# Kernel optimization log

Measured on AMD Instinct MI355X. Metric: run time of the kernel, lower is better.

## Reference

```python
import jax, jax.numpy as jnp
import numpy as np

E = 1024
H = 16
N, S, T = 4, 2048, 2048


def setup_inputs() -> dict:
    key = jax.random.key(0)
    ks = jax.random.split(key, 11)
    scale = 1.0 / np.sqrt(E)
    inp = {
        "query": jax.random.normal(ks[0], (N, S, E), jnp.float32),
        "key": jax.random.normal(ks[1], (N, T, E), jnp.float32),
        "value": jax.random.normal(ks[2], (N, T, E), jnp.float32),
        "Wq": jax.random.normal(ks[3], (E, E), jnp.float32) * scale,
        "bq": jax.random.normal(ks[4], (E,), jnp.float32) * 0.01,
        "Wk": jax.random.normal(ks[5], (E, E), jnp.float32) * scale,
        "bk": jax.random.normal(ks[6], (E,), jnp.float32) * 0.01,
        "Wv": jax.random.normal(ks[7], (E, E), jnp.float32) * scale,
        "bv": jax.random.normal(ks[8], (E,), jnp.float32) * 0.01,
        "Wp": jax.random.normal(ks[9], (E, E), jnp.float32) * scale,
        "bp": jax.random.normal(ks[10], (E,), jnp.float32) * 0.01,
    }
    return inp


def reference(query, key, value, Wq, bq, Wk, bk, Wv, bv, Wp, bp):
    n, s, e = query.shape
    t = value.shape[1]
    hd = e // H
    # Linear projections (torch Linear: x @ W^T + b), split into heads -> [N,H,S,hd]
    Q = (query @ Wq.T + bq).reshape(n, s, H, hd).transpose(0, 2, 1, 3)
    K = (key @ Wk.T + bk).reshape(n, t, H, hd).transpose(0, 2, 1, 3)
    V = (value @ Wv.T + bv).reshape(n, t, H, hd).transpose(0, 2, 1, 3)
    scale = 1.0 / jnp.sqrt(jnp.asarray(hd, Q.dtype))
    attn = jnp.einsum("nhsd,nhtd->nhst", Q, K) * scale  # [N,H,S,T]
    A = jax.nn.softmax(attn, axis=-1)
    Y = jnp.einsum("nhst,nhtd->nhsd", A, V)  # [N,H,S,hd]
    Y = Y.transpose(0, 2, 1, 3).reshape(n, s, e)
    return Y @ Wp.T + bp
```

## Files before the change

kernel.cpp:

```cpp
#include <hip/hip_runtime.h>
#include <hip/hip_bf16.h>
#include <stdint.h>


#define E_DIM 1024
#define H_NUM 16
#define HD 64
#define NB 4
#define SEQ 2048
#define NTOK (NB * SEQ)

typedef __bf16 bf16x8 __attribute__((ext_vector_type(8)));
typedef float f32x4 __attribute__((ext_vector_type(4)));
typedef float f32x16 __attribute__((ext_vector_type(16)));
typedef unsigned short u16;

#define MFMA16(a, b, c) __builtin_amdgcn_mfma_f32_16x16x32_bf16(a, b, c, 0, 0, 0)
#define MFMA32(a, b, c) __builtin_amdgcn_mfma_f32_32x32x16_bf16(a, b, c, 0, 0, 0)

#define VMCNT(n) asm volatile("s_waitcnt vmcnt(" #n ")" ::: "memory")
#define BAR() __builtin_amdgcn_s_barrier()
#define PRIO1() __builtin_amdgcn_s_setprio(1)
#define PRIO0() __builtin_amdgcn_s_setprio(0)

__device__ __forceinline__ u16 f2bf(float f) {
  unsigned int u = __builtin_bit_cast(unsigned int, f);
  unsigned int r = (u + 0x7FFFu + ((u >> 16) & 1u)) >> 16;
  return (u16)r;
}

__device__ __forceinline__ float fexp2(float x) {
  return __builtin_amdgcn_exp2f(x);
}

__device__ __forceinline__ void gload_lds16(const void* g, void* l) {
  __builtin_amdgcn_global_load_lds((const __attribute__((address_space(1))) void*)g,
                                   (__attribute__((address_space(3))) void*)l,
                                   16, 0, 0);
}

__device__ __forceinline__ unsigned cvtpk(float lo, float hi2) {
  unsigned w;
  asm("v_cvt_pk_bf16_f32 %0, %1, %2" : "=v"(w) : "v"(lo), "v"(hi2));
  return w;
}
__device__ __forceinline__ void plswap(unsigned& a, unsigned& b) {
  asm("v_permlane32_swap_b32 %0, %1" : "+v"(a), "+v"(b));
}

__global__ __launch_bounds__(256) void cvt7(const float* __restrict__ s0,
                                            const float* __restrict__ s1,
                                            const float* __restrict__ s2,
                                            const float* __restrict__ s3,
                                            const float* __restrict__ s4,
                                            const float* __restrict__ s5,
                                            const float* __restrict__ s6,
                                            u16* d0, u16* d1, u16* d2, u16* d3,
                                            u16* d4, u16* d5, u16* d6,
                                            int nbig, int nsmall) {
  const int t = blockIdx.y;
  const float* in;
  u16* out;
  int n4;
  switch (t) {
    case 0: in = s0; out = d0; n4 = nbig; break;
    case 1: in = s1; out = d1; n4 = nbig; break;
    case 2: in = s2; out = d2; n4 = nbig; break;
    case 3: in = s3; out = d3; n4 = nsmall; break;
    case 4: in = s4; out = d4; n4 = nsmall; break;
    case 5: in = s5; out = d5; n4 = nsmall; break;
    default: in = s6; out = d6; n4 = nsmall; break;
  }
  int idx = blockIdx.x * 256 + threadIdx.x;
  int stride = gridDim.x * 256;
  for (int i = idx; i < n4; i += stride) {
    float4 v = ((const float4*)in)[i];
    ushort4 o;
    o.x = f2bf(v.x); o.y = f2bf(v.y); o.z = f2bf(v.z); o.w = f2bf(v.w);
    ((ushort4*)out)[i] = o;
  }
}


__device__ __forceinline__ void rdA(bf16x8 (&af)[4][2], const char* pA, int off) {
#pragma unroll
  for (int mi = 0; mi < 4; mi++)
#pragma unroll
    for (int kk = 0; kk < 2; kk++)
      af[mi][kk] = *(const bf16x8*)(pA + off + mi * 2048 + kk * 64);
}
__device__ __forceinline__ void rdB(bf16x8 (&bfr)[2][2], const char* pB, int off) {
#pragma unroll
  for (int nj = 0; nj < 2; nj++)
#pragma unroll
    for (int kk = 0; kk < 2; kk++)
      bfr[nj][kk] = *(const bf16x8*)(pB + off + nj * 2048 + kk * 64);
}
template <int MI0, int NJ0>
__device__ __forceinline__ void mm16(f32x4 (&acc)[8][4], bf16x8 (&af)[4][2],
                                     bf16x8 (&bfr)[2][2]) {
#pragma unroll
  for (int kk = 0; kk < 2; kk++)
#pragma unroll
    for (int mi = 0; mi < 4; mi++)
#pragma unroll
      for (int nj = 0; nj < 2; nj++)
        acc[MI0 + mi][NJ0 + nj] = MFMA16(af[mi][kk], bfr[nj][kk], acc[MI0 + mi][NJ0 + nj]);
}

__global__ void __launch_bounds__(512, 2) gemm_qkv8(
    const u16* __restrict__ qb, const u16* __restrict__ kb, const u16* __restrict__ vb,
    const u16* __restrict__ Wcat, const float* __restrict__ bq,
    const float* __restrict__ bk, const float* __restrict__ bv,
    u16* __restrict__ Qp, u16* __restrict__ Kp, u16* __restrict__ Vt, float qscale) {
  extern __shared__ char LDS[];
  const int tid = threadIdx.x;
  const int w = tid >> 6, l = tid & 63;
  const int lr = l & 15, lg = l >> 4;
  const int wr = w >> 2, wc2 = w & 3;
  const int m0 = blockIdx.y * 256;
  const int n0g = blockIdx.x * 256;
  const int z = blockIdx.x >> 2;
  const u16* A = (z == 0) ? qb : (z == 1) ? kb : vb;

  const int colsw = (lg << 4) ^ ((lr & 4) << 3);
  const char* pA = LDS + (wr * 16384 + lr * 128 + colsw);
  const char* pB = LDS + (65536 + (wc2 >> 1) * 16384 + ((wc2 & 1) * 64 + lr) * 128 + colsw);

  const int sr0 = tid >> 3;
  const int sc = (((tid & 7) * 16) ^ ((sr0 & 4) << 3)) >> 1;
  const u16* aS[2];
  const u16* bS[2];
#pragma unroll
  for (int ld = 0; ld < 2; ld++) {
    aS[ld] = A + (size_t)(m0 + ld * 64 + sr0) * E_DIM + sc;
    bS[ld] = Wcat + (size_t)(n0g + ld * 64 + sr0) * E_DIM + sc;
  }

#define STG_A(h, kt)                                                                   \
  do {                                                                                 \
    const int _b = (kt) & 1;                                                           \
    gload_lds16(aS[0] + (h) * 131072 + (size_t)(kt) * 64,                              \
                LDS + _b * 32768 + (h) * 16384 + w * 1024);                            \
    gload_lds16(aS[1] + (h) * 131072 + (size_t)(kt) * 64,                              \
                LDS + _b * 32768 + (h) * 16384 + w * 1024 + 8192);                     \
  } while (0)
#define STG_B(h, kt)                                                                   \
  do {                                                                                 \
    const int _b = (kt) & 1;                                                           \
    gload_lds16(bS[0] + (h) * 131072 + (size_t)(kt) * 64,                              \
                LDS + 65536 + _b * 32768 + (h) * 16384 + w * 1024);                    \
    gload_lds16(bS[1] + (h) * 131072 + (size_t)(kt) * 64,                              \
                LDS + 65536 + _b * 32768 + (h) * 16384 + w * 1024 + 8192);             \
  } while (0)

  f32x4 acc[8][4] = {};
  bf16x8 af[4][2], bfr[2][2];

#define FRAME(T, LAST)                                                                 \
  do {                                                                                 \
                                                             \
    rdA(af, pA, 0); rdB(bfr, pB, 0);                                                   \
    STG_B(0, (T) + 1);                                                                 \
    BAR(); PRIO1(); mm16<0, 0>(acc, af, bfr); PRIO0(); BAR();                          \
                                                                     \
    rdB(bfr, pB, 4096);                                                                \
    STG_B(1, (T) + 1);                                                                 \
    BAR(); PRIO1(); mm16<0, 2>(acc, af, bfr); PRIO0(); BAR();                          \
                                                                     \
    rdA(af, pA, 8192);                                                                 \
    STG_A(1, (T) + 1);                                                                 \
    BAR(); PRIO1(); mm16<4, 2>(acc, af, bfr); PRIO0(); BAR();                          \
                                                             \
    rdB(bfr, pB, 0);                                                                   \
    if (!(LAST)) { STG_A(0, (T) + 2); VMCNT(2); } else { VMCNT(0); }                   \
    BAR(); PRIO1(); mm16<4, 0>(acc, af, bfr); PRIO0(); BAR();                          \
                                                     \
    rdA(af, pA, 32768); rdB(bfr, pB, 32768);                                           \
    if (!(LAST)) STG_B(0, (T) + 2);                                                    \
    BAR(); PRIO1(); mm16<0, 0>(acc, af, bfr); PRIO0(); BAR();                          \
                                                                     \
    rdB(bfr, pB, 32768 + 4096);                                                        \
    if (!(LAST)) STG_B(1, (T) + 2);                                                    \
    BAR(); PRIO1(); mm16<0, 2>(acc, af, bfr); PRIO0(); BAR();                          \
                                                                     \
    rdA(af, pA, 32768 + 8192);                                                         \
    if (!(LAST)) STG_A(1, (T) + 2);                                                    \
    BAR(); PRIO1(); mm16<4, 2>(acc, af, bfr); PRIO0(); BAR();                          \
                                                             \
    rdB(bfr, pB, 32768);                                                               \
    if (!(LAST)) { STG_A(0, (T) + 3); VMCNT(2); }                                      \
    BAR(); PRIO1(); mm16<4, 0>(acc, af, bfr); PRIO0(); BAR();                          \
  } while (0)

  STG_A(0, 0); STG_A(1, 0); STG_B(0, 0); STG_B(1, 0); STG_A(0, 1);
  VMCNT(2);
  BAR();

#pragma unroll 1
  for (int T = 0; T < 14; T += 2) FRAME(T, false);
  FRAME(14, true);

  const float* bias = (z == 0) ? bq : (z == 1) ? bk : bv;
  const float osc = (z == 0) ? qscale : 1.0f;
#pragma unroll
  for (int mi = 0; mi < 8; mi++) {
#pragma unroll
    for (int nj = 0; nj < 4; nj++) {
      const int colm = (n0g + wc2 * 64 + nj * 16 + lr) & 1023;
      const float bvv = bias[colm];
      const int row0 = m0 + wr * 128 + mi * 16 + lg * 4;
      if (z == 2) {
        const int nb = row0 >> 11, t = row0 & (SEQ - 1);
        const int hh = colm >> 6, d = colm & 63;
        ushort4 o;
        o.x = f2bf(acc[mi][nj][0] + bvv);
        o.y = f2bf(acc[mi][nj][1] + bvv);
        o.z = f2bf(acc[mi][nj][2] + bvv);
        o.w = f2bf(acc[mi][nj][3] + bvv);
        *(ushort4*)&Vt[(((size_t)((nb * H_NUM + hh) * HD + d)) << 11) + t] = o;
      } else {
        u16* Cb = (z == 0) ? Qp : Kp;
#pragma unroll
        for (int ri = 0; ri < 4; ri++)
          Cb[(size_t)(row0 + ri) * E_DIM + colm] = f2bf((acc[mi][nj][ri] + bvv) * osc);
      }
    }
  }
#undef FRAME
#undef STG_A
#undef STG_B
}

__global__ __launch_bounds__(256) void gemm_proj(const u16* __restrict__ A,
                                                 const u16* __restrict__ W,
                                                 const float* __restrict__ bias,
                                                 float* __restrict__ Cout) {
  __shared__ u16 As[2][128 * 32];
  __shared__ u16 Bs[2][128 * 32];
  const int tid = threadIdx.x;
  const int w = tid >> 6, l = tid & 63;
  const int lg = l >> 4, lr = l & 15;
  const int m0 = blockIdx.y * 128, n0 = blockIdx.x * 128;
  const int wr = (w >> 1) * 64, wc = (w & 1) * 64;
  f32x4 acc[4][4] = {};
  const int qa0 = w, qa1 = 4 + w;
  const int rowA0 = qa0 * 16 + (l >> 2), rowA1 = qa1 * 16 + (l >> 2);
  const int colA = (l & 3) * 8;
  const u16* aptr0 = A + (size_t)(m0 + rowA0) * E_DIM + colA;
  const u16* aptr1 = A + (size_t)(m0 + rowA1) * E_DIM + colA;
  const u16* bptr0 = W + (size_t)(n0 + rowA0) * E_DIM + colA;
  const u16* bptr1 = W + (size_t)(n0 + rowA1) * E_DIM + colA;

#define GSTAGE(B, k0)                                   \
  do {                                                  \
    gload_lds16(aptr0 + (k0), &As[B][qa0 * 512]);       \
    gload_lds16(aptr1 + (k0), &As[B][qa1 * 512]);       \
    gload_lds16(bptr0 + (k0), &Bs[B][qa0 * 512]);       \
    gload_lds16(bptr1 + (k0), &Bs[B][qa1 * 512]);       \
  } while (0)
#define GBODY(B)                                                          \
  do {                                                                    \
    bf16x8 af[4], bfr[4];                                                 \
    _Pragma("unroll") for (int mi = 0; mi < 4; mi++)                      \
      af[mi] = *(const bf16x8*)&As[B][(wr + mi * 16 + lr) * 32 + lg * 8]; \
    _Pragma("unroll") for (int nj = 0; nj < 4; nj++)                      \
      bfr[nj] = *(const bf16x8*)&Bs[B][(wc + nj * 16 + lr) * 32 + lg * 8];\
    _Pragma("unroll") for (int mi = 0; mi < 4; mi++)                      \
      _Pragma("unroll") for (int nj = 0; nj < 4; nj++)                    \
        acc[mi][nj] = MFMA16(af[mi], bfr[nj], acc[mi][nj]);               \
  } while (0)

  GSTAGE(0, 0);
  __syncthreads();
#pragma unroll 1
  for (int k0 = 0; k0 < E_DIM; k0 += 64) {
    GSTAGE(1, k0 + 32);
    GBODY(0);
    __syncthreads();
    if (k0 + 64 < E_DIM) GSTAGE(0, k0 + 64);
    GBODY(1);
    __syncthreads();
  }
#pragma unroll
  for (int mi = 0; mi < 4; mi++) {
#pragma unroll
    for (int nj = 0; nj < 4; nj++) {
      const int col = n0 + wc + nj * 16 + lr;
      const float bv = bias[col];
      const int row0 = m0 + wr + mi * 16 + lg * 4;
#pragma unroll
      for (int ri = 0; ri < 4; ri++)
        Cout[(size_t)(row0 + ri) * E_DIM + col] = acc[mi][nj][ri] + bv;
    }
  }
#undef GSTAGE
#undef GBODY
}

__global__ __launch_bounds__(256) void attn_kernel(const u16* __restrict__ Qp,
                                                   const u16* __restrict__ Kp,
                                                   const u16* __restrict__ Vt,
                                                   u16* __restrict__ Yb) {
  __shared__ u16 Ks[2][64 * 64];
  __shared__ u16 Vs[2][64 * 64];
  const int h = blockIdx.x, qt = blockIdx.y, n = blockIdx.z;
  const int tid = threadIdx.x;
  const int w = tid >> 6, l = tid & 63;
  const int c = l & 31, hi = l >> 5;
  const int q0 = qt * 128 + w * 32;

  bf16x8 qf[4];
  {
    const u16* qrow = Qp + (size_t)(n * SEQ + q0 + c) * E_DIM + h * HD + hi * 8;
#pragma unroll
    for (int ks = 0; ks < 4; ks++) qf[ks] = *(const bf16x8*)(qrow + ks * 16);
  }

  f32x16 y0 = {}, y1 = {};
  float lrun = 0.f;

  int lo[4];
#pragma unroll
  for (int ks = 0; ks < 4; ks++)
    lo[ks] = c * 128 + ((ks * 32 + hi * 16) ^ ((c & 7) << 4));

  const int sr = l >> 3;
  const int sc = ((l & 7) ^ sr) * 8;
  const u16* kgb[2];
  const u16* vgb[2];
#pragma unroll
  for (int g = 0; g < 2; g++) {
    const int row_ = (w << 4) + (g << 3) + sr;
    kgb[g] = Kp + (size_t)(n * SEQ + row_) * E_DIM + h * HD + sc;
    vgb[g] = Vt + ((size_t)((n * H_NUM + h) * HD + row_)) * SEQ + sc;
  }

#define STAGE(B, t0)                                                    \
  do {                                                                  \
    gload_lds16(kgb[0] + (size_t)(t0) * E_DIM, &Ks[B][(w << 10)]);      \
    gload_lds16(kgb[1] + (size_t)(t0) * E_DIM, &Ks[B][(w << 10) + 512]);\
    gload_lds16(vgb[0] + (t0), &Vs[B][(w << 10)]);                      \
    gload_lds16(vgb[1] + (t0), &Vs[B][(w << 10) + 512]);                \
  } while (0)

#define TILE_BODY(B)                                                           \
  do {                                                                         \
    const char* kb = (const char*)Ks[B];                                       \
    const char* vb = (const char*)Vs[B];                                       \
    f32x16 s0 = {}, s1 = {};                                                   \
    PRIO1();                                                                   \
    _Pragma("unroll") for (int ks = 0; ks < 4; ks++) {                         \
      bf16x8 ka0 = *(const bf16x8*)(kb + lo[ks]);                              \
      bf16x8 ka1 = *(const bf16x8*)(kb + lo[ks] + 4096);                       \
      s0 = MFMA32(ka0, qf[ks], s0);                                            \
      s1 = MFMA32(ka1, qf[ks], s1);                                            \
    }                                                                          \
    PRIO0();                                                                   \
    float p0 = 0.f, p1 = 0.f, p2 = 0.f, p3 = 0.f;                              \
    _Pragma("unroll") for (int r = 0; r < 4; r++) {                            \
      s0[r] = fexp2(s0[r]);         p0 += s0[r];                               \
      s0[r + 4] = fexp2(s0[r + 4]); p1 += s0[r + 4];                           \
      s0[r + 8] = fexp2(s0[r + 8]); p2 += s0[r + 8];                           \
      s0[r + 12] = fexp2(s0[r + 12]); p3 += s0[r + 12];                        \
    }                                                                          \
    _Pragma("unroll") for (int r = 0; r < 4; r++) {                            \
      s1[r] = fexp2(s1[r]);         p0 += s1[r];                               \
      s1[r + 4] = fexp2(s1[r + 4]); p1 += s1[r + 4];                           \
      s1[r + 8] = fexp2(s1[r + 8]); p2 += s1[r + 8];                           \
      s1[r + 12] = fexp2(s1[r + 12]); p3 += s1[r + 12];                        \
    }                                                                          \
    lrun += (p0 + p1) + (p2 + p3);                                             \
    PRIO1();                                                                   \
    _Pragma("unroll") for (int ks = 0; ks < 4; ks++) {                         \
      const f32x16 pe = (ks < 2) ? s0 : s1;                                    \
      const int b0 = (ks & 1) * 8;                                             \
      unsigned wa = cvtpk(pe[b0 + 0], pe[b0 + 1]);                             \
      unsigned wb = cvtpk(pe[b0 + 4], pe[b0 + 5]);                             \
      unsigned wc2 = cvtpk(pe[b0 + 2], pe[b0 + 3]);                            \
      unsigned wd = cvtpk(pe[b0 + 6], pe[b0 + 7]);                             \
      plswap(wa, wb);                                                          \
      plswap(wc2, wd);                                                         \
      union { unsigned u[4]; bf16x8 v; } pa;                                   \
      pa.u[0] = wa; pa.u[1] = wc2; pa.u[2] = wb; pa.u[3] = wd;                 \
      bf16x8 va0 = *(const bf16x8*)(vb + lo[ks]);                              \
      bf16x8 va1 = *(const bf16x8*)(vb + lo[ks] + 4096);                       \
      y0 = MFMA32(va0, pa.v, y0);                                              \
      y1 = MFMA32(va1, pa.v, y1);                                              \
    }                                                                          \
    PRIO0();                                                                   \
  } while (0)

  STAGE(0, 0);
  __syncthreads();

#pragma unroll 1
  for (int it = 0; it < SEQ / 64; it += 2) {
    STAGE(1, (it + 1) * 64);
    TILE_BODY(0);
    __syncthreads();
    if (it + 2 < SEQ / 64) STAGE(0, (it + 2) * 64);
    TILE_BODY(1);
    __syncthreads();
  }

  lrun += __shfl_xor(lrun, 32, 64);
  const float inv = 1.f / lrun;
  u16* orow = Yb + (size_t)(n * SEQ + q0 + c) * E_DIM + h * HD;
#pragma unroll
  for (int df = 0; df < 2; df++) {
    const f32x16 yy = df ? y1 : y0;
#pragma unroll
    for (int g = 0; g < 4; g++) {
      ushort4 o;
      o.x = f2bf(yy[g * 4 + 0] * inv);
      o.y = f2bf(yy[g * 4 + 1] * inv);
      o.z = f2bf(yy[g * 4 + 2] * inv);
      o.w = f2bf(yy[g * 4 + 3] * inv);
      *(ushort4*)(orow + df * 32 + g * 8 + hi * 4) = o;
    }
  }
#undef STAGE
#undef TILE_BODY
}

extern "C" void kernel_launch(void* const* d_in, const int* in_sizes, int n_in,
                              void* d_out, int out_size, void* d_ws, size_t ws_size,
                              hipStream_t stream) {
  const float* query = (const float*)d_in[0];
  const float* key   = (const float*)d_in[1];
  const float* value = (const float*)d_in[2];
  const float* Wq = (const float*)d_in[3];
  const float* bq = (const float*)d_in[4];
  const float* Wk = (const float*)d_in[5];
  const float* bk = (const float*)d_in[6];
  const float* Wv = (const float*)d_in[7];
  const float* bv = (const float*)d_in[8];
  const float* Wp = (const float*)d_in[9];
  const float* bp = (const float*)d_in[10];

  const size_t TOK_E = (size_t)NTOK * E_DIM;
  const size_t W_E = (size_t)E_DIM * E_DIM;

  u16* ws = (u16*)d_ws;
  u16* qb  = ws;
  u16* kb  = qb + TOK_E;
  u16* vb  = kb + TOK_E;
  u16* wqb = vb + TOK_E;
  u16* wkb = wqb + W_E;
  u16* wvb = wkb + W_E;
  u16* wpb = wvb + W_E;
  u16* Qp  = wpb + W_E;
  u16* Kp  = Qp + TOK_E;
  u16* Vtb = Kp + TOK_E;
  u16* Yb  = Vtb + TOK_E;

  cvt7<<<dim3(1024, 7), 256, 0, stream>>>(query, key, value, Wq, Wk, Wv, Wp,
                                          qb, kb, vb, wqb, wkb, wvb, wpb,
                                          (int)(TOK_E / 4), (int)(W_E / 4));

  const float sc2 = 0.125f * 1.44269504088896f;

  hipFuncSetAttribute((const void*)gemm_qkv8,
                      hipFuncAttributeMaxDynamicSharedMemorySize, 131072);
  gemm_qkv8<<<dim3(3072 / 256, NTOK / 256), 512, 131072, stream>>>(
      qb, kb, vb, wqb, bq, bk, bv, Qp, Kp, Vtb, sc2);

  attn_kernel<<<dim3(H_NUM, SEQ / 128, NB), 256, 0, stream>>>(Qp, Kp, Vtb, Yb);

  gemm_proj<<<dim3(E_DIM / 128, NTOK / 128), 256, 0, stream>>>(Yb, wpb, bp, (float*)d_out);
}
```

Measured before the change: 218.5 us.

## Process two 32-row query subtiles per wave in attention kernel to reuse K/V

Each wave in the attention kernel now handles 64 query rows, as two 32-row sets, instead of 32. Each K and V fragment read from LDS feeds four MFMAs instead of two, and the grid is halved to 256 queries per block. This halves LDS and global K/V traffic per query and amortizes staging and barriers. The cost is roughly double the accumulator registers, a launch bound of 2 blocks per CU, and fewer blocks (512) to spread across CUs, which may reduce occupancy.

```diff
diff --git a/kernel.cpp b/kernel.cpp
--- a/kernel.cpp
+++ b/kernel.cpp
@@ -46,6 +46,19 @@
 }
 __device__ __forceinline__ void plswap(unsigned& a, unsigned& b) {
   asm("v_permlane32_swap_b32 %0, %1" : "+v"(a), "+v"(b));
+}
+
+template <int B0>
+__device__ __forceinline__ bf16x8 packpa(const f32x16& pe) {
+  unsigned wa = cvtpk(pe[B0 + 0], pe[B0 + 1]);
+  unsigned wb = cvtpk(pe[B0 + 4], pe[B0 + 5]);
+  unsigned wc2 = cvtpk(pe[B0 + 2], pe[B0 + 3]);
+  unsigned wd = cvtpk(pe[B0 + 6], pe[B0 + 7]);
+  plswap(wa, wb);
+  plswap(wc2, wd);
+  union { unsigned u[4]; bf16x8 v; } pa;
+  pa.u[0] = wa; pa.u[1] = wc2; pa.u[2] = wb; pa.u[3] = wd;
+  return pa.v;
 }
 
 __global__ __launch_bounds__(256) void cvt7(const float* __restrict__ s0,
@@ -81,7 +94,6 @@
   }
 }
 
-
 __device__ __forceinline__ void rdA(bf16x8 (&af)[4][2], const char* pA, int off) {
 #pragma unroll
   for (int mi = 0; mi < 4; mi++)
@@ -159,35 +171,27 @@
 
 #define FRAME(T, LAST)                                                                 \
   do {                                                                                 \
-                                                             \
     rdA(af, pA, 0); rdB(bfr, pB, 0);                                                   \
     STG_B(0, (T) + 1);                                                                 \
     BAR(); PRIO1(); mm16<0, 0>(acc, af, bfr); PRIO0(); BAR();                          \
-                                                                     \
     rdB(bfr, pB, 4096);                                                                \
     STG_B(1, (T) + 1);                                                                 \
     BAR(); PRIO1(); mm16<0, 2>(acc, af, bfr); PRIO0(); BAR();                          \
-                                                                     \
     rdA(af, pA, 8192);                                                                 \
     STG_A(1, (T) + 1);                                                                 \
     BAR(); PRIO1(); mm16<4, 2>(acc, af, bfr); PRIO0(); BAR();                          \
-                                                             \
     rdB(bfr, pB, 0);                                                                   \
     if (!(LAST)) { STG_A(0, (T) + 2); VMCNT(2); } else { VMCNT(0); }                   \
     BAR(); PRIO1(); mm16<4, 0>(acc, af, bfr); PRIO0(); BAR();                          \
-                                                     \
     rdA(af, pA, 32768); rdB(bfr, pB, 32768);                                           \
     if (!(LAST)) STG_B(0, (T) + 2);                                                    \
     BAR(); PRIO1(); mm16<0, 0>(acc, af, bfr); PRIO0(); BAR();                          \
-                                                                     \
     rdB(bfr, pB, 32768 + 4096);                                                        \
     if (!(LAST)) STG_B(1, (T) + 2);                                                    \
     BAR(); PRIO1(); mm16<0, 2>(acc, af, bfr); PRIO0(); BAR();                          \
-                                                                     \
     rdA(af, pA, 32768 + 8192);                                                         \
     if (!(LAST)) STG_A(1, (T) + 2);                                                    \
     BAR(); PRIO1(); mm16<4, 2>(acc, af, bfr); PRIO0(); BAR();                          \
-                                                             \
     rdB(bfr, pB, 32768);                                                               \
     if (!(LAST)) { STG_A(0, (T) + 3); VMCNT(2); }                                      \
     BAR(); PRIO1(); mm16<4, 0>(acc, af, bfr); PRIO0(); BAR();                          \
@@ -298,27 +302,31 @@
 #undef GBODY
 }
 
-__global__ __launch_bounds__(256) void attn_kernel(const u16* __restrict__ Qp,
-                                                   const u16* __restrict__ Kp,
-                                                   const u16* __restrict__ Vt,
-                                                   u16* __restrict__ Yb) {
+__global__ __launch_bounds__(256, 2) void attn_kernel(const u16* __restrict__ Qp,
+                                                      const u16* __restrict__ Kp,
+                                                      const u16* __restrict__ Vt,
+                                                      u16* __restrict__ Yb) {
   __shared__ u16 Ks[2][64 * 64];
   __shared__ u16 Vs[2][64 * 64];
   const int h = blockIdx.x, qt = blockIdx.y, n = blockIdx.z;
   const int tid = threadIdx.x;
   const int w = tid >> 6, l = tid & 63;
   const int c = l & 31, hi = l >> 5;
-  const int q0 = qt * 128 + w * 32;
-
-  bf16x8 qf[4];
+  const int q0 = qt * 256 + w * 64;
+
+  bf16x8 qfA[4], qfB[4];
   {
-    const u16* qrow = Qp + (size_t)(n * SEQ + q0 + c) * E_DIM + h * HD + hi * 8;
-#pragma unroll
-    for (int ks = 0; ks < 4; ks++) qf[ks] = *(const bf16x8*)(qrow + ks * 16);
-  }
-
-  f32x16 y0 = {}, y1 = {};
-  float lrun = 0.f;
+    const u16* qrowA = Qp + (size_t)(n * SEQ + q0 + c) * E_DIM + h * HD + hi * 8;
+    const u16* qrowB = qrowA + 32 * E_DIM;
+#pragma unroll
+    for (int ks = 0; ks < 4; ks++) {
+      qfA[ks] = *(const bf16x8*)(qrowA + ks * 16);
+      qfB[ks] = *(const bf16x8*)(qrowB + ks * 16);
+    }
+  }
+
+  f32x16 yA0 = {}, yA1 = {}, yB0 = {}, yB1 = {};
+  float lrA = 0.f, lrB = 0.f;
 
   int lo[4];
 #pragma unroll
@@ -348,45 +356,43 @@
   do {                                                                         \
     const char* kb = (const char*)Ks[B];                                       \
     const char* vb = (const char*)Vs[B];                                       \
-    f32x16 s0 = {}, s1 = {};                                                   \
+    f32x16 sA0 = {}, sA1 = {}, sB0 = {}, sB1 = {};                             \
     PRIO1();                                                                   \
     _Pragma("unroll") for (int ks = 0; ks < 4; ks++) {                         \
       bf16x8 ka0 = *(const bf16x8*)(kb + lo[ks]);                              \
       bf16x8 ka1 = *(const bf16x8*)(kb + lo[ks] + 4096);                       \
-      s0 = MFMA32(ka0, qf[ks], s0);                                            \
-      s1 = MFMA32(ka1, qf[ks], s1);                                            \
+      sA0 = MFMA32(ka0, qfA[ks], sA0);                                         \
+      sA1 = MFMA32(ka1, qfA[ks], sA1);                                         \
+      sB0 = MFMA32(ka0, qfB[ks], sB0);                                         \
+      sB1 = MFMA32(ka1, qfB[ks], sB1);                                         \
     }                                                                          \
     PRIO0();                                                                   \
-    float p0 = 0.f, p1 = 0.f, p2 = 0.f, p3 = 0.f;                              \
-    _Pragma("unroll") for (int r = 0; r < 4; r++) {                            \
-      s0[r] = fexp2(s0[r]);         p0 += s0[r];                               \
-      s0[r + 4] = fexp2(s0[r + 4]); p1 += s0[r + 4];                           \
-      s0[r + 8] = fexp2(s0[r + 8]); p2 += s0[r + 8];                           \
-      s0[r + 12] = fexp2(s0[r + 12]); p3 += s0[r + 12];                        \
+    float pa0 = 0.f, pa1 = 0.f, pb0 = 0.f, pb1 = 0.f;                          \
+    _Pragma("unroll") for (int r = 0; r < 8; r++) {                            \
+      sA0[r] = fexp2(sA0[r]);         pa0 += sA0[r];                           \
+      sA0[r + 8] = fexp2(sA0[r + 8]); pa1 += sA0[r + 8];                       \
+      sA1[r] = fexp2(sA1[r]);         pa0 += sA1[r];                           \
+      sA1[r + 8] = fexp2(sA1[r + 8]); pa1 += sA1[r + 8];                       \
+      sB0[r] = fexp2(sB0[r]);         pb0 += sB0[r];                           \
+      sB0[r + 8] = fexp2(sB0[r + 8]); pb1 += sB0[r + 8];                       \
+      sB1[r] = fexp2(sB1[r]);         pb0 += sB1[r];                           \
+      sB1[r + 8] = fexp2(sB1[r + 8]); pb1 += sB1[r + 8];                       \
     }                                                                          \
-    _Pragma("unroll") for (int r = 0; r < 4; r++) {                            \
-      s1[r] = fexp2(s1[r]);         p0 += s1[r];                               \
-      s1[r + 4] = fexp2(s1[r + 4]); p1 += s1[r + 4];                           \
-      s1[r + 8] = fexp2(s1[r + 8]); p2 += s1[r + 8];                           \
-      s1[r + 12] = fexp2(s1[r + 12]); p3 += s1[r + 12];                        \
-    }                                                                          \
-    lrun += (p0 + p1) + (p2 + p3);                                             \
+    lrA += pa0 + pa1;                                                          \
+    lrB += pb0 + pb1;                                                          \
     PRIO1();                                                                   \
     _Pragma("unroll") for (int ks = 0; ks < 4; ks++) {                         \
-      const f32x16 pe = (ks < 2) ? s0 : s1;                                    \
-      const int b0 = (ks & 1) * 8;                                             \
-      unsigned wa = cvtpk(pe[b0 + 0], pe[b0 + 1]);                             \
-      unsigned wb = cvtpk(pe[b0 + 4], pe[b0 + 5]);                             \
-      unsigned wc2 = cvtpk(pe[b0 + 2], pe[b0 + 3]);                            \
-      unsigned wd = cvtpk(pe[b0 + 6], pe[b0 + 7]);                             \
-      plswap(wa, wb);                                                          \
-      plswap(wc2, wd);                                                         \
-      union { unsigned u[4]; bf16x8 v; } pa;                                   \
-      pa.u[0] = wa; pa.u[1] = wc2; pa.u[2] = wb; pa.u[3] = wd;                 \
+      const f32x16& peA = (ks < 2) ? sA0 : sA1;                                \
+      const f32x16& peB = (ks < 2) ? sB0 : sB1;                                \
+      bf16x8 paA, paB;                                                         \
+      if (ks & 1) { paA = packpa<8>(peA); paB = packpa<8>(peB); }              \
+      else        { paA = packpa<0>(peA); paB = packpa<0>(peB); }              \
       bf16x8 va0 = *(const bf16x8*)(vb + lo[ks]);                              \
       bf16x8 va1 = *(const bf16x8*)(vb + lo[ks] + 4096);                       \
-      y0 = MFMA32(va0, pa.v, y0);                                              \
-      y1 = MFMA32(va1, pa.v, y1);                                              \
+      yA0 = MFMA32(va0, paA, yA0);                                             \
+      yA1 = MFMA32(va1, paA, yA1);                                             \
+      yB0 = MFMA32(va0, paB, yB0);                                             \
+      yB1 = MFMA32(va1, paB, yB1);                                             \
     }                                                                          \
     PRIO0();                                                                   \
   } while (0)
@@ -404,20 +410,29 @@
     __syncthreads();
   }
 
-  lrun += __shfl_xor(lrun, 32, 64);
-  const float inv = 1.f / lrun;
-  u16* orow = Yb + (size_t)(n * SEQ + q0 + c) * E_DIM + h * HD;
+  lrA += __shfl_xor(lrA, 32, 64);
+  lrB += __shfl_xor(lrB, 32, 64);
+  const float invA = 1.f / lrA;
+  const float invB = 1.f / lrB;
+  u16* orowA = Yb + (size_t)(n * SEQ + q0 + c) * E_DIM + h * HD;
+  u16* orowB = orowA + (size_t)32 * E_DIM;
 #pragma unroll
   for (int df = 0; df < 2; df++) {
-    const f32x16 yy = df ? y1 : y0;
+    const f32x16 ya = df ? yA1 : yA0;
+    const f32x16 yb2 = df ? yB1 : yB0;
 #pragma unroll
     for (int g = 0; g < 4; g++) {
-      ushort4 o;
-      o.x = f2bf(yy[g * 4 + 0] * inv);
-      o.y = f2bf(yy[g * 4 + 1] * inv);
-      o.z = f2bf(yy[g * 4 + 2] * inv);
-      o.w = f2bf(yy[g * 4 + 3] * inv);
-      *(ushort4*)(orow + df * 32 + g * 8 + hi * 4) = o;
+      ushort4 oA, oB;
+      oA.x = f2bf(ya[g * 4 + 0] * invA);
+      oA.y = f2bf(ya[g * 4 + 1] * invA);
+      oA.z = f2bf(ya[g * 4 + 2] * invA);
+      oA.w = f2bf(ya[g * 4 + 3] * invA);
+      oB.x = f2bf(yb2[g * 4 + 0] * invB);
+      oB.y = f2bf(yb2[g * 4 + 1] * invB);
+      oB.z = f2bf(yb2[g * 4 + 2] * invB);
+      oB.w = f2bf(yb2[g * 4 + 3] * invB);
+      *(ushort4*)(orowA + df * 32 + g * 8 + hi * 4) = oA;
+      *(ushort4*)(orowB + df * 32 + g * 8 + hi * 4) = oB;
     }
   }
 #undef STAGE
@@ -466,7 +481,7 @@
   gemm_qkv8<<<dim3(3072 / 256, NTOK / 256), 512, 131072, stream>>>(
       qb, kb, vb, wqb, bq, bk, bv, Qp, Kp, Vtb, sc2);
 
-  attn_kernel<<<dim3(H_NUM, SEQ / 128, NB), 256, 0, stream>>>(Qp, Kp, Vtb, Yb);
+  attn_kernel<<<dim3(H_NUM, SEQ / 256, NB), 256, 0, stream>>>(Qp, Kp, Vtb, Yb);
 
   gemm_proj<<<dim3(E_DIM / 128, NTOK / 128), 256, 0, stream>>>(Yb, wpb, bp, (float*)d_out);
 }
```

Result: faster. 203.4 us (-6.9%).
